# Optimization experiments

Hardware: AMD Instinct MI355X
Metric: run time of the kernel (lower is better)

## Reference

```python
import jax, jax.numpy as jnp
import numpy as np

N, IN_DIM, HID, H1, NCLS, H2, E = 50000, 256, 32, 8, 16, 8, 800000


def gat_conv(x, edge_index, W, a_src, a_dst, b, H, C):
    """PyG-style GATConv, eval mode (attention dropout off), concat=True,
    negative_slope=0.2, add_self_loops=True."""
    n = x.shape[0]
    loop = jnp.arange(n)
    src = jnp.concatenate([edge_index[0], loop])  # [E+N]
    dst = jnp.concatenate([edge_index[1], loop])
    h = (x @ W).reshape(n, H, C)                  # [N,H,C]
    alpha_s = jnp.sum(h * a_src, axis=-1)         # [N,H]
    alpha_d = jnp.sum(h * a_dst, axis=-1)         # [N,H]
    e = jax.nn.leaky_relu(alpha_s[src] + alpha_d[dst], 0.2)  # [E+N,H]
    # segment softmax over incoming edges of each target node
    e_max = jax.ops.segment_max(e, dst, num_segments=n)      # [N,H] (self-loop guarantees nonempty)
    p = jnp.exp(e - e_max[dst])
    denom = jax.ops.segment_sum(p, dst, num_segments=n)
    alpha = p / (denom[dst] + 1e-16)              # [E+N,H]
    msg = h[src] * alpha[:, :, None]              # [E+N,H,C]
    out = jax.ops.segment_sum(msg, dst, num_segments=n)      # [N,H,C]
    return out.reshape(n, H * C) + b


def setup_inputs() -> dict:
    key = jax.random.key(0)
    ks = jax.random.split(key, 12)
    x = jax.random.normal(ks[0], (N, IN_DIM), dtype=jnp.float32)
    edge_index = jax.random.randint(ks[1], (2, E), 0, N, dtype=jnp.int64)
    s1 = 1.0 / np.sqrt(IN_DIM)
    s2 = 1.0 / np.sqrt(HID * H1)
    W1 = jax.random.normal(ks[2], (IN_DIM, H1 * HID), dtype=jnp.float32) * s1
    a_src1 = jax.random.normal(ks[3], (H1, HID), dtype=jnp.float32) * s1
    a_dst1 = jax.random.normal(ks[4], (H1, HID), dtype=jnp.float32) * s1
    b1 = jnp.zeros((H1 * HID,), dtype=jnp.float32)
    W2 = jax.random.normal(ks[5], (H1 * HID, H2 * NCLS), dtype=jnp.float32) * s2
    a_src2 = jax.random.normal(ks[6], (H2, NCLS), dtype=jnp.float32) * s2
    a_dst2 = jax.random.normal(ks[7], (H2, NCLS), dtype=jnp.float32) * s2
    b2 = jnp.zeros((H2 * NCLS,), dtype=jnp.float32)
    return {"x": x, "edge_index": edge_index, "W1": W1, "a_src1": a_src1,
            "a_dst1": a_dst1, "b1": b1, "W2": W2, "a_src2": a_src2,
            "a_dst2": a_dst2, "b2": b2}


def reference(x, edge_index, W1, a_src1, a_dst1, b1, W2, a_src2, a_dst2, b2):
    # eval mode: F.dropout is identity
    h = gat_conv(x, edge_index, W1, a_src1, a_dst1, b1, H1, HID)   # [N, H1*HID]
    h = jax.nn.elu(h)
    h = gat_conv(h, edge_index, W2, a_src2, a_dst2, b2, H2, NCLS)  # [N, H2*NCLS]
    return jax.nn.log_softmax(h, axis=1)
```

## Files before the change

### kernel.cpp

```cpp
#include <hip/hip_runtime.h>
#include <hip/hip_fp16.h>

#define NN 50000
#define NE 800000

typedef _Float16 half4v __attribute__((ext_vector_type(4)));
typedef _Float16 half8v __attribute__((ext_vector_type(8)));
typedef float f32x4 __attribute__((ext_vector_type(4)));

#define Q_SCALE 0.04724409448f
#define Q_INV   21.16666667f

#define CVTB0(f, w) asm("v_cvt_f32_ubyte0 %0, %1" : "=v"(f) : "v"(w))
#define CVTB1(f, w) asm("v_cvt_f32_ubyte1 %0, %1" : "=v"(f) : "v"(w))
#define CVTB2(f, w) asm("v_cvt_f32_ubyte2 %0, %1" : "=v"(f) : "v"(w))
#define CVTB3(f, w) asm("v_cvt_f32_ubyte3 %0, %1" : "=v"(f) : "v"(w))

static __device__ __forceinline__ float lrelu(float x) { return x > 0.f ? x : 0.2f * x; }

static __device__ __forceinline__ int detect64(const void* ei) {
  const unsigned* w = (const unsigned*)ei;
  return (w[1] | w[3] | w[5] | w[7]) == 0u;
}

static __device__ __forceinline__ int edge_at(const void* ei, int is64, long long idx) {
  if (is64) return (int)((const long long*)ei)[idx];
  return ((const int*)ei)[idx];
}

__global__ void count_prep_kernel(const void* __restrict__ ei, int* __restrict__ counts,
                                  const float* __restrict__ W1, const float* __restrict__ W2,
                                  const float* __restrict__ aS1, const float* __restrict__ aD1,
                                  const float* __restrict__ aS2, const float* __restrict__ aD2,
                                  _Float16* __restrict__ W1p, _Float16* __restrict__ W2p,
                                  _Float16* __restrict__ Wa1p, _Float16* __restrict__ Wa2p) {
  long long gid = (long long)blockIdx.x * blockDim.x + threadIdx.x;
  if (gid < NE) {
    int is64 = detect64(ei);
    int d = edge_at(ei, is64, (long long)NE + gid);
    atomicAdd(&counts[d], 1);
    return;
  }
  int i = (int)(gid - NE);
  if (i < 65536) {
    int j = i & 7, l = (i >> 3) & 63, kst = (i >> 9) & 7, ct = i >> 12;
    int col = ct * 16 + (l & 15);
    int k = kst * 32 + ((l >> 4) << 3) + j;
    W1p[i] = (_Float16)W1[(size_t)k * 256 + col];
  } else if (i < 98304) {
    int n = i - 65536;
    int j = n & 7, l = (n >> 3) & 63, kst = (n >> 9) & 7, ct = n >> 12;
    int col = ct * 16 + (l & 15);
    int k = kst * 32 + ((l >> 4) << 3) + j;
    W2p[n] = (_Float16)W2[(size_t)k * 128 + col];
  } else if (i < 102400) {
    int n = i - 98304;
    int j = n & 7, l = (n >> 3) & 63, kst = n >> 9;
    int row = l & 15;
    int head = row & 7;
    const float* a = (row < 8) ? aS1 : aD1;
    int k = kst * 32 + ((l >> 4) << 3) + j;
    float s = 0.f;
    #pragma unroll 8
    for (int c = 0; c < 32; ++c)
      s += W1[(size_t)k * 256 + head * 32 + c] * a[head * 32 + c];
    Wa1p[n] = (_Float16)s;
  } else if (i < 106496) {
    int n = i - 102400;
    int j = n & 7, l = (n >> 3) & 63, kst = n >> 9;
    int row = l & 15;
    int head = row & 7;
    const float* a = (row < 8) ? aS2 : aD2;
    int k = kst * 32 + ((l >> 4) << 3) + j;
    float s = 0.f;
    #pragma unroll 8
    for (int c = 0; c < 16; ++c)
      s += W2[(size_t)k * 128 + head * 16 + c] * a[head * 16 + c];
    Wa2p[n] = (_Float16)s;
  }
}

static __device__ __forceinline__ int block_scan_inc(int v, int tid) {
  __shared__ int ws[4];
  const int lane = tid & 63, wv = tid >> 6;
  #pragma unroll
  for (int off = 1; off < 64; off <<= 1) {
    int t = __shfl_up(v, off);
    if (lane >= off) v += t;
  }
  if (lane == 63) ws[wv] = v;
  __syncthreads();
  int add = 0;
  #pragma unroll
  for (int j = 0; j < 4; ++j) if (j < wv) add += ws[j];
  return v + add;
}

__global__ void scan1_kernel(const int* __restrict__ counts, int* __restrict__ bsums) {
  __shared__ int ws[4];
  const int tid = threadIdx.x;
  const int lane = tid & 63, wv = tid >> 6;
  int i = blockIdx.x * 256 + tid;
  int v = (i < NN) ? counts[i] : 0;
  #pragma unroll
  for (int off = 1; off < 64; off <<= 1) v += __shfl_xor(v, off);
  if (lane == 0) ws[wv] = v;
  __syncthreads();
  if (tid == 0) bsums[blockIdx.x] = ws[0] + ws[1] + ws[2] + ws[3];
}

__global__ void scan2_kernel(int* __restrict__ bsums, int nb) {
  const int tid = threadIdx.x;
  int v = (tid < nb) ? bsums[tid] : 0;
  int inc = block_scan_inc(v, tid);
  if (tid < nb) bsums[tid] = inc - v;
}

__global__ void scan3_kernel(const int* __restrict__ counts, const int* __restrict__ bsums,
                             int* __restrict__ rs) {
  const int tid = threadIdx.x;
  int i = blockIdx.x * 256 + tid;
  int v = (i < NN) ? counts[i] : 0;
  int inc = block_scan_inc(v, tid);
  if (i < NN) rs[i + 1] = bsums[blockIdx.x] + inc;
  if (i == 0) rs[0] = 0;
}

__global__ void scatter_kernel(const void* __restrict__ ei,
                               const int* __restrict__ rs, int* __restrict__ cursor,
                               int* __restrict__ ssrc) {
  int e = blockIdx.x * blockDim.x + threadIdx.x;
  if (e >= NE) return;
  int is64 = detect64(ei);
  int s = edge_at(ei, is64, e);
  int d = edge_at(ei, is64, (long long)NE + e);
  int p = atomicAdd(&cursor[d], 1);
  ssrc[rs[d] + p] = s;
}

template<int BN, int NCF, bool A_Q8, bool Q8OUT>
__global__ __launch_bounds__(512) void gemm_mfma(const void* __restrict__ Araw,
                                                 const _Float16* __restrict__ Bp,
                                                 const _Float16* __restrict__ Wap,
                                                 void* __restrict__ Cout,
                                                 float* __restrict__ alS,
                                                 float* __restrict__ alD, int M) {
  __shared__ __align__(16) _Float16 As[64][256 + 8];
  const int tid = threadIdx.x;
  const int bm0 = blockIdx.x * 64;
  if (A_Q8) {
    const unsigned char* A8 = (const unsigned char*)Araw;
    #pragma unroll
    for (int t = 0; t < 2; ++t) {
      int idx = tid + t * 512;
      int r = idx >> 4, c16 = (idx & 15) << 4;
      int gr = bm0 + r;
      uint4 v = make_uint4(0x80808080u, 0x80808080u, 0x80808080u, 0x80808080u);
      if (gr < M) v = *(const uint4*)&A8[(size_t)gr * 256 + c16];
      unsigned dw[4] = { v.x, v.y, v.z, v.w };
      _Float16 hb[16];
      #pragma unroll
      for (int d = 0; d < 4; ++d) {
        float f0, f1, f2, f3;
        CVTB0(f0, dw[d]); CVTB1(f1, dw[d]); CVTB2(f2, dw[d]); CVTB3(f3, dw[d]);
        hb[4 * d + 0] = (_Float16)((f0 - 128.f) * Q_SCALE);
        hb[4 * d + 1] = (_Float16)((f1 - 128.f) * Q_SCALE);
        hb[4 * d + 2] = (_Float16)((f2 - 128.f) * Q_SCALE);
        hb[4 * d + 3] = (_Float16)((f3 - 128.f) * Q_SCALE);
      }
      *(half8v*)&As[r][c16] = *(half8v*)&hb[0];
      *(half8v*)&As[r][c16 + 8] = *(half8v*)&hb[8];
    }
  } else {
    const float* A = (const float*)Araw;
    #pragma unroll
    for (int g = 0; g < 2; ++g) {
      float4 tmp[4]; int rr[4], cc[4];
      #pragma unroll
      for (int t = 0; t < 4; ++t) {
        int idx = tid + (g * 4 + t) * 512;
        int r = idx >> 6, c4 = (idx & 63) << 2;
        int gr = bm0 + r;
        tmp[t] = make_float4(0.f, 0.f, 0.f, 0.f);
        if (gr < M) tmp[t] = *(const float4*)&A[(size_t)gr * 256 + c4];
        rr[t] = r; cc[t] = c4;
      }
      #pragma unroll
      for (int t = 0; t < 4; ++t) {
        half4v h = { (_Float16)tmp[t].x, (_Float16)tmp[t].y,
                     (_Float16)tmp[t].z, (_Float16)tmp[t].w };
        *(half4v*)&As[rr[t]][cc[t]] = h;
      }
    }
  }
  __syncthreads();
  const int lane = tid & 63, wv = tid >> 6;
  const int ncol0 = wv * (16 * NCF);
  const int lrow = lane & 15, lk8 = (lane >> 4) << 3;
  f32x4 acc[4][NCF];
  f32x4 acca[4];
  #pragma unroll
  for (int rf = 0; rf < 4; ++rf) {
    acca[rf] = (f32x4){0.f, 0.f, 0.f, 0.f};
    #pragma unroll
    for (int cf = 0; cf < NCF; ++cf) acc[rf][cf] = (f32x4){0.f, 0.f, 0.f, 0.f};
  }
  #pragma unroll
  for (int kst = 0; kst < 8; ++kst) {
    const int ks = kst * 32 + lk8;
    half8v af[4];
    #pragma unroll
    for (int rf = 0; rf < 4; ++rf)
      af[rf] = *(const half8v*)&As[16 * rf + lrow][ks];
    #pragma unroll
    for (int cf = 0; cf < NCF; ++cf) {
      half8v bf = *(const half8v*)&Bp[((size_t)((wv * NCF + cf) * 8 + kst) * 64 + lane) * 8];
      #pragma unroll
      for (int rf = 0; rf < 4; ++rf)
        acc[rf][cf] = __builtin_amdgcn_mfma_f32_16x16x32_f16(af[rf], bf, acc[rf][cf], 0, 0, 0);
    }
    if (wv == 0) {
      half8v bfa = *(const half8v*)&Wap[((size_t)kst * 64 + lane) * 8];
      #pragma unroll
      for (int rf = 0; rf < 4; ++rf)
        acca[rf] = __builtin_amdgcn_mfma_f32_16x16x32_f16(af[rf], bfa, acca[rf], 0, 0, 0);
    }
  }
  if (Q8OUT) {
    __syncthreads();
    constexpr int ROWB = BN + 16;
    char* Cs = (char*)&As[0][0];
    #pragma unroll
    for (int rf = 0; rf < 4; ++rf) {
      #pragma unroll
      for (int j = 0; j < 4; ++j) {
        int r = 16 * rf + 4 * ((lane >> 4) & 3) + j;
        #pragma unroll
        for (int cf = 0; cf < NCF; ++cf) {
          int col = ncol0 + 16 * cf + lrow;
          float v = acc[rf][cf][j];
          int q = __float2int_rn(fminf(fmaxf(v * Q_INV, -127.f), 127.f)) + 128;
          Cs[r * ROWB + col] = (char)q;
        }
      }
    }
    __syncthreads();
    unsigned char* C8 = (unsigned char*)Cout;
    for (int idx = tid; idx < 4 * BN; idx += 512) {
      int r = idx / (BN / 16), c16 = idx % (BN / 16);
      int grow = bm0 + r;
      if (grow < M)
        *(int4*)&C8[(size_t)grow * BN + 16 * c16] = *(const int4*)&Cs[r * ROWB + 16 * c16];
    }
  }
  if (wv == 0) {
    #pragma unroll
    for (int rf = 0; rf < 4; ++rf) {
      #pragma unroll
      for (int j = 0; j < 4; ++j) {
        int row = bm0 + 16 * rf + 4 * ((lane >> 4) & 3) + j;
        if (row < M) {
          float v = acca[rf][j];
          if (lrow < 8) alS[row * 8 + lrow] = v;
          else          alD[row * 8 + (lrow - 8)] = v;
        }
      }
    }
  }
}

#define ACCQ(w, p) do { \
    float f0_, f1_, f2_, f3_; \
    CVTB0(f0_, (w)); CVTB1(f1_, (w)); CVTB2(f2_, (w)); CVTB3(f3_, (w)); \
    ax0 += (p) * f0_; ax1 += (p) * f1_; ax2 += (p) * f2_; ax3 += (p) * f3_; \
  } while (0)

__global__ __launch_bounds__(256) void agg1_kernel(const unsigned char* __restrict__ h1q,
    const float* __restrict__ as, const float* __restrict__ ad,
    const int* __restrict__ rs, const int* __restrict__ ssrc,
    const float* __restrict__ bias, unsigned char* __restrict__ outq) {
  const int wid = (blockIdx.x * blockDim.x + threadIdx.x) >> 6;
  const int lane = threadIdx.x & 63;
  if (wid >= NN) return;
  const int node = wid;
  const int beg = rs[node], end = rs[node + 1];
  const int deg = end - beg;
  const int hd = lane >> 3;
  const float advh = ad[node * 8 + hd];
  const unsigned* hw = (const unsigned*)h1q;
  float denom = 0.f;
  float ax0 = 0.f, ax1 = 0.f, ax2 = 0.f, ax3 = 0.f;
  {
    float p = __expf(lrelu(as[node * 8 + hd] + advh));
    unsigned w = hw[(size_t)node * 64 + lane];
    ACCQ(w, p);
    denom = p;
  }
  const int gb = lane & 56;
  for (int base = 0; base < deg; base += 64) {
    const int cnt = min(deg - base, 64);
    int sv = (lane < cnt) ? ssrc[beg + base + lane] : 0;
    int j = 0;
    for (; j + 8 <= cnt; j += 8) {
      int s0 = __builtin_amdgcn_readlane(sv, j + 0);
      int s1 = __builtin_amdgcn_readlane(sv, j + 1);
      int s2 = __builtin_amdgcn_readlane(sv, j + 2);
      int s3 = __builtin_amdgcn_readlane(sv, j + 3);
      int s4 = __builtin_amdgcn_readlane(sv, j + 4);
      int s5 = __builtin_amdgcn_readlane(sv, j + 5);
      int s6 = __builtin_amdgcn_readlane(sv, j + 6);
      int s7 = __builtin_amdgcn_readlane(sv, j + 7);
      unsigned w0 = hw[(size_t)s0 * 64 + lane];
      unsigned w1 = hw[(size_t)s1 * 64 + lane];
      unsigned w2 = hw[(size_t)s2 * 64 + lane];
      unsigned w3 = hw[(size_t)s3 * 64 + lane];
      unsigned w4 = hw[(size_t)s4 * 64 + lane];
      unsigned w5 = hw[(size_t)s5 * 64 + lane];
      unsigned w6 = hw[(size_t)s6 * 64 + lane];
      unsigned w7 = hw[(size_t)s7 * 64 + lane];
      int sl = __shfl(sv, j + (lane & 7));
      float pl = __expf(lrelu(as[(size_t)sl * 8 + hd] + advh));
      float p0 = __shfl(pl, gb + 0);
      float p1 = __shfl(pl, gb + 1);
      float p2 = __shfl(pl, gb + 2);
      float p3 = __shfl(pl, gb + 3);
      float p4 = __shfl(pl, gb + 4);
      float p5 = __shfl(pl, gb + 5);
      float p6 = __shfl(pl, gb + 6);
      float p7 = __shfl(pl, gb + 7);
      denom += (p0 + p1) + (p2 + p3) + ((p4 + p5) + (p6 + p7));
      ACCQ(w0, p0); ACCQ(w1, p1); ACCQ(w2, p2); ACCQ(w3, p3);
      ACCQ(w4, p4); ACCQ(w5, p5); ACCQ(w6, p6); ACCQ(w7, p7);
    }
    for (; j < cnt; ++j) {
      int s = __builtin_amdgcn_readlane(sv, j);
      float p = __expf(lrelu(as[s * 8 + hd] + advh));
      unsigned w = hw[(size_t)s * 64 + lane];
      ACCQ(w, p);
      denom += p;
    }
  }
  const float inv = 1.f / (denom + 1e-16f);
  const float4 bv = *(const float4*)&bias[lane * 4];
  float4 o;
  o.x = Q_SCALE * (ax0 * inv - 128.f) + bv.x;
  o.y = Q_SCALE * (ax1 * inv - 128.f) + bv.y;
  o.z = Q_SCALE * (ax2 * inv - 128.f) + bv.z;
  o.w = Q_SCALE * (ax3 * inv - 128.f) + bv.w;
  o.x = o.x > 0.f ? o.x : __expf(o.x) - 1.f;
  o.y = o.y > 0.f ? o.y : __expf(o.y) - 1.f;
  o.z = o.z > 0.f ? o.z : __expf(o.z) - 1.f;
  o.w = o.w > 0.f ? o.w : __expf(o.w) - 1.f;
  int q0 = __float2int_rn(fminf(fmaxf(o.x * Q_INV, -127.f), 127.f)) + 128;
  int q1 = __float2int_rn(fminf(fmaxf(o.y * Q_INV, -127.f), 127.f)) + 128;
  int q2 = __float2int_rn(fminf(fmaxf(o.z * Q_INV, -127.f), 127.f)) + 128;
  int q3 = __float2int_rn(fminf(fmaxf(o.w * Q_INV, -127.f), 127.f)) + 128;
  unsigned pk = (unsigned)q0 | ((unsigned)q1 << 8) | ((unsigned)q2 << 16) | ((unsigned)q3 << 24);
  ((unsigned*)outq)[(size_t)node * 64 + lane] = pk;
}

#define ACC2Q(w, p) do { \
    float f0_, f1_; \
    CVTB0(f0_, (w)); CVTB1(f1_, (w)); \
    ax0 += (p) * f0_; ax1 += (p) * f1_; \
  } while (0)

__global__ __launch_bounds__(256) void agg2_kernel(const unsigned char* __restrict__ h2q,
    const float* __restrict__ as, const float* __restrict__ ad,
    const int* __restrict__ rs, const int* __restrict__ ssrc,
    const float* __restrict__ bias, float* __restrict__ out) {
  const int wid = (blockIdx.x * blockDim.x + threadIdx.x) >> 6;
  const int lane = threadIdx.x & 63;
  if (wid >= NN) return;
  const int node = wid;
  const int beg = rs[node], end = rs[node + 1];
  const int deg = end - beg;
  const int hd = lane >> 3;
  const float advh = ad[node * 8 + hd];
  const unsigned short* hw = (const unsigned short*)h2q;
  float denom = 0.f;
  float ax0 = 0.f, ax1 = 0.f;
  {
    float p = __expf(lrelu(as[node * 8 + hd] + advh));
    unsigned w = hw[(size_t)node * 64 + lane];
    ACC2Q(w, p);
    denom = p;
  }
  const int gb = lane & 56;
  for (int base = 0; base < deg; base += 64) {
    const int cnt = min(deg - base, 64);
    int sv = (lane < cnt) ? ssrc[beg + base + lane] : 0;
    int j = 0;
    for (; j + 8 <= cnt; j += 8) {
      int s0 = __builtin_amdgcn_readlane(sv, j + 0);
      int s1 = __builtin_amdgcn_readlane(sv, j + 1);
      int s2 = __builtin_amdgcn_readlane(sv, j + 2);
      int s3 = __builtin_amdgcn_readlane(sv, j + 3);
      int s4 = __builtin_amdgcn_readlane(sv, j + 4);
      int s5 = __builtin_amdgcn_readlane(sv, j + 5);
      int s6 = __builtin_amdgcn_readlane(sv, j + 6);
      int s7 = __builtin_amdgcn_readlane(sv, j + 7);
      unsigned w0 = hw[(size_t)s0 * 64 + lane];
      unsigned w1 = hw[(size_t)s1 * 64 + lane];
      unsigned w2 = hw[(size_t)s2 * 64 + lane];
      unsigned w3 = hw[(size_t)s3 * 64 + lane];
      unsigned w4 = hw[(size_t)s4 * 64 + lane];
      unsigned w5 = hw[(size_t)s5 * 64 + lane];
      unsigned w6 = hw[(size_t)s6 * 64 + lane];
      unsigned w7 = hw[(size_t)s7 * 64 + lane];
      int sl = __shfl(sv, j + (lane & 7));
      float pl = __expf(lrelu(as[(size_t)sl * 8 + hd] + advh));
      float p0 = __shfl(pl, gb + 0);
      float p1 = __shfl(pl, gb + 1);
      float p2 = __shfl(pl, gb + 2);
      float p3 = __shfl(pl, gb + 3);
      float p4 = __shfl(pl, gb + 4);
      float p5 = __shfl(pl, gb + 5);
      float p6 = __shfl(pl, gb + 6);
      float p7 = __shfl(pl, gb + 7);
      denom += (p0 + p1) + (p2 + p3) + ((p4 + p5) + (p6 + p7));
      ACC2Q(w0, p0); ACC2Q(w1, p1); ACC2Q(w2, p2); ACC2Q(w3, p3);
      ACC2Q(w4, p4); ACC2Q(w5, p5); ACC2Q(w6, p6); ACC2Q(w7, p7);
    }
    for (; j < cnt; ++j) {
      int s = __builtin_amdgcn_readlane(sv, j);
      float p = __expf(lrelu(as[s * 8 + hd] + advh));
      unsigned w = hw[(size_t)s * 64 + lane];
      ACC2Q(w, p);
      denom += p;
    }
  }
  const float inv = 1.f / (denom + 1e-16f);
  float v0 = Q_SCALE * (ax0 * inv - 128.f) + bias[lane * 2 + 0];
  float v1 = Q_SCALE * (ax1 * inv - 128.f) + bias[lane * 2 + 1];
  float mx = fmaxf(v0, v1);
  #pragma unroll
  for (int off = 1; off < 64; off <<= 1) mx = fmaxf(mx, __shfl_xor(mx, off));
  float sum = __expf(v0 - mx) + __expf(v1 - mx);
  #pragma unroll
  for (int off = 1; off < 64; off <<= 1) sum += __shfl_xor(sum, off);
  float lse = mx + __logf(sum);
  float2 o = make_float2(v0 - lse, v1 - lse);
  __builtin_nontemporal_store(o.x, &out[(size_t)node * 128 + lane * 2]);
  __builtin_nontemporal_store(o.y, &out[(size_t)node * 128 + lane * 2 + 1]);
}

extern "C" void kernel_launch(void* const* d_in, const int* in_sizes, int n_in,
                              void* d_out, int out_size, void* d_ws, size_t ws_size,
                              hipStream_t stream) {
  const float* x    = (const float*)d_in[0];
  const void*  ei   = d_in[1];
  const float* W1   = (const float*)d_in[2];
  const float* aS1  = (const float*)d_in[3];
  const float* aD1  = (const float*)d_in[4];
  const float* b1   = (const float*)d_in[5];
  const float* W2   = (const float*)d_in[6];
  const float* aS2  = (const float*)d_in[7];
  const float* aD2  = (const float*)d_in[8];
  const float* b2   = (const float*)d_in[9];
  float* out = (float*)d_out;

  char* ws = (char*)d_ws;
  unsigned char* h1q = (unsigned char*)ws; ws += (size_t)NN * 256;
  unsigned char* hmq = (unsigned char*)ws; ws += (size_t)NN * 256;
  unsigned char* h2q = (unsigned char*)ws; ws += (size_t)NN * 128;
  _Float16* W1p = (_Float16*)ws;       ws += (size_t)65536 * 2;
  _Float16* W2p = (_Float16*)ws;       ws += (size_t)32768 * 2;
  _Float16* Wa1p = (_Float16*)ws;      ws += (size_t)4096 * 2;
  _Float16* Wa2p = (_Float16*)ws;      ws += (size_t)4096 * 2;
  float* alS  = (float*)ws;            ws += (size_t)NN * 8 * 4;
  float* alD  = (float*)ws;            ws += (size_t)NN * 8 * 4;
  int* counts = (int*)ws;              ws += (size_t)NN * 4;
  int* cursor = (int*)ws;              ws += (size_t)NN * 4;
  int* rs     = (int*)ws;              ws += (size_t)(NN + 1) * 4;
  int* bsums  = (int*)ws;              ws += (size_t)256 * 4;
  int* ssrc   = (int*)ws;              ws += (size_t)NE * 4;

  const int NB = (NN + 255) / 256;

  hipMemsetAsync(counts, 0, (size_t)2 * NN * 4, stream);

  const long long total_cp = (long long)NE + 106496;
  count_prep_kernel<<<(int)((total_cp + 255) / 256), 256, 0, stream>>>(
      ei, counts, W1, W2, aS1, aD1, aS2, aD2, W1p, W2p, Wa1p, Wa2p);

  scan1_kernel<<<NB, 256, 0, stream>>>(counts, bsums);
  scan2_kernel<<<1, 256, 0, stream>>>(bsums, NB);
  scan3_kernel<<<NB, 256, 0, stream>>>(counts, bsums, rs);
  scatter_kernel<<<(NE + 255) / 256, 256, 0, stream>>>(ei, rs, cursor, ssrc);

  const int ngrid = (NN + 63) / 64;
  gemm_mfma<256, 2, false, true><<<ngrid, 512, 0, stream>>>(x, W1p, Wa1p, h1q, alS, alD, NN);
  agg1_kernel<<<(NN + 3) / 4, 256, 0, stream>>>(h1q, alS, alD, rs, ssrc, b1, hmq);

  gemm_mfma<128, 1, true, true><<<ngrid, 512, 0, stream>>>(hmq, W2p, Wa2p, h2q, alS, alD, NN);
  agg2_kernel<<<(NN + 3) / 4, 256, 0, stream>>>(h2q, alS, alD, rs, ssrc, b2, out);
}
```

Baseline: 215.6 us.

## Fuse edge scatter into layer-1 GEMM launch and store sources as 16-bit

Merges the CSR scatter kernel into the first GEMM launch by appending extra blocks that do the edge scatter, so the two independent jobs run concurrently in one grid instead of back to back. It also shrinks the sorted source-index array from 32-bit to 16-bit, halving the index traffic in scatter and both aggregation kernels. The 16-bit indices can only hold values up to 65535, which is enough for 50000 nodes but hardcodes that limit. The shared-memory GEMM body now lives in a device function, and scatter blocks share the 512-thread launch bounds.

```diff
diff --git a/kernel.cpp b/kernel.cpp
--- a/kernel.cpp
+++ b/kernel.cpp
@@ -3,6 +3,7 @@
 
 #define NN 50000
 #define NE 800000
+#define NGRID1 782
 
 typedef _Float16 half4v __attribute__((ext_vector_type(4)));
 typedef _Float16 half8v __attribute__((ext_vector_type(8)));
@@ -126,20 +127,8 @@
   if (i == 0) rs[0] = 0;
 }
 
-__global__ void scatter_kernel(const void* __restrict__ ei,
-                               const int* __restrict__ rs, int* __restrict__ cursor,
-                               int* __restrict__ ssrc) {
-  int e = blockIdx.x * blockDim.x + threadIdx.x;
-  if (e >= NE) return;
-  int is64 = detect64(ei);
-  int s = edge_at(ei, is64, e);
-  int d = edge_at(ei, is64, (long long)NE + e);
-  int p = atomicAdd(&cursor[d], 1);
-  ssrc[rs[d] + p] = s;
-}
-
 template<int BN, int NCF, bool A_Q8, bool Q8OUT>
-__global__ __launch_bounds__(512) void gemm_mfma(const void* __restrict__ Araw,
+static __device__ __forceinline__ void gemm_body(int bid, const void* __restrict__ Araw,
                                                  const _Float16* __restrict__ Bp,
                                                  const _Float16* __restrict__ Wap,
                                                  void* __restrict__ Cout,
@@ -147,7 +136,7 @@
                                                  float* __restrict__ alD, int M) {
   __shared__ __align__(16) _Float16 As[64][256 + 8];
   const int tid = threadIdx.x;
-  const int bm0 = blockIdx.x * 64;
+  const int bm0 = bid * 64;
   if (A_Q8) {
     const unsigned char* A8 = (const unsigned char*)Araw;
     #pragma unroll
@@ -269,6 +258,32 @@
   }
 }
 
+__global__ __launch_bounds__(512) void gemm1_scatter_kernel(
+    const void* __restrict__ Araw, const _Float16* __restrict__ Bp,
+    const _Float16* __restrict__ Wap, void* __restrict__ Cout,
+    float* __restrict__ alS, float* __restrict__ alD, int M,
+    const void* __restrict__ ei, const int* __restrict__ rs,
+    int* __restrict__ cursor, unsigned short* __restrict__ ssrc) {
+  if (blockIdx.x < NGRID1) {
+    gemm_body<256, 2, false, true>(blockIdx.x, Araw, Bp, Wap, Cout, alS, alD, M);
+    return;
+  }
+  int e = (blockIdx.x - NGRID1) * 512 + threadIdx.x;
+  if (e >= NE) return;
+  int is64 = detect64(ei);
+  int s = edge_at(ei, is64, e);
+  int d = edge_at(ei, is64, (long long)NE + e);
+  int p = atomicAdd(&cursor[d], 1);
+  ssrc[rs[d] + p] = (unsigned short)s;
+}
+
+__global__ __launch_bounds__(512) void gemm2_kernel(
+    const void* __restrict__ Araw, const _Float16* __restrict__ Bp,
+    const _Float16* __restrict__ Wap, void* __restrict__ Cout,
+    float* __restrict__ alS, float* __restrict__ alD, int M) {
+  gemm_body<128, 1, true, true>(blockIdx.x, Araw, Bp, Wap, Cout, alS, alD, M);
+}
+
 #define ACCQ(w, p) do { \
     float f0_, f1_, f2_, f3_; \
     CVTB0(f0_, (w)); CVTB1(f1_, (w)); CVTB2(f2_, (w)); CVTB3(f3_, (w)); \
@@ -277,7 +292,7 @@
 
 __global__ __launch_bounds__(256) void agg1_kernel(const unsigned char* __restrict__ h1q,
     const float* __restrict__ as, const float* __restrict__ ad,
-    const int* __restrict__ rs, const int* __restrict__ ssrc,
+    const int* __restrict__ rs, const unsigned short* __restrict__ ssrc,
     const float* __restrict__ bias, unsigned char* __restrict__ outq) {
   const int wid = (blockIdx.x * blockDim.x + threadIdx.x) >> 6;
   const int lane = threadIdx.x & 63;
@@ -299,7 +314,7 @@
   const int gb = lane & 56;
   for (int base = 0; base < deg; base += 64) {
     const int cnt = min(deg - base, 64);
-    int sv = (lane < cnt) ? ssrc[beg + base + lane] : 0;
+    int sv = (lane < cnt) ? (int)ssrc[beg + base + lane] : 0;
     int j = 0;
     for (; j + 8 <= cnt; j += 8) {
       int s0 = __builtin_amdgcn_readlane(sv, j + 0);
@@ -367,7 +382,7 @@
 
 __global__ __launch_bounds__(256) void agg2_kernel(const unsigned char* __restrict__ h2q,
     const float* __restrict__ as, const float* __restrict__ ad,
-    const int* __restrict__ rs, const int* __restrict__ ssrc,
+    const int* __restrict__ rs, const unsigned short* __restrict__ ssrc,
     const float* __restrict__ bias, float* __restrict__ out) {
   const int wid = (blockIdx.x * blockDim.x + threadIdx.x) >> 6;
   const int lane = threadIdx.x & 63;
@@ -389,7 +404,7 @@
   const int gb = lane & 56;
   for (int base = 0; base < deg; base += 64) {
     const int cnt = min(deg - base, 64);
-    int sv = (lane < cnt) ? ssrc[beg + base + lane] : 0;
+    int sv = (lane < cnt) ? (int)ssrc[beg + base + lane] : 0;
     int j = 0;
     for (; j + 8 <= cnt; j += 8) {
       int s0 = __builtin_amdgcn_readlane(sv, j + 0);
@@ -474,7 +489,7 @@
   int* cursor = (int*)ws;              ws += (size_t)NN * 4;
   int* rs     = (int*)ws;              ws += (size_t)(NN + 1) * 4;
   int* bsums  = (int*)ws;              ws += (size_t)256 * 4;
-  int* ssrc   = (int*)ws;              ws += (size_t)NE * 4;
+  unsigned short* ssrc = (unsigned short*)ws; ws += (size_t)NE * 2;
 
   const int NB = (NN + 255) / 256;
 
@@ -487,12 +502,13 @@
   scan1_kernel<<<NB, 256, 0, stream>>>(counts, bsums);
   scan2_kernel<<<1, 256, 0, stream>>>(bsums, NB);
   scan3_kernel<<<NB, 256, 0, stream>>>(counts, bsums, rs);
-  scatter_kernel<<<(NE + 255) / 256, 256, 0, stream>>>(ei, rs, cursor, ssrc);
-
-  const int ngrid = (NN + 63) / 64;
-  gemm_mfma<256, 2, false, true><<<ngrid, 512, 0, stream>>>(x, W1p, Wa1p, h1q, alS, alD, NN);
+
+  const int sgrid = (NE + 511) / 512;
+  gemm1_scatter_kernel<<<NGRID1 + sgrid, 512, 0, stream>>>(
+      x, W1p, Wa1p, h1q, alS, alD, NN, ei, rs, cursor, ssrc);
+
   agg1_kernel<<<(NN + 3) / 4, 256, 0, stream>>>(h1q, alS, alD, rs, ssrc, b1, hmq);
 
-  gemm_mfma<128, 1, true, true><<<ngrid, 512, 0, stream>>>(hmq, W2p, Wa2p, h2q, alS, alD, NN);
+  gemm2_kernel<<<NGRID1, 512, 0, stream>>>(hmq, W2p, Wa2p, h2q, alS, alD, NN);
   agg2_kernel<<<(NN + 3) / 4, 256, 0, stream>>>(h2q, alS, alD, rs, ssrc, b2, out);
 }
```

Result: faster. 197.2 us (median of 2 runs) (-8.5%).
